# Kernel tuning notes

Hardware: AMD Instinct MI355X
Metric: run time of the kernel (lower is better)

## Reference

```python
import jax, jax.numpy as jnp
import numpy as np

B, K2, C, H, W = 8, 9, 1, 256, 1216


def setup_inputs() -> dict:
    key = jax.random.key(0)
    k1, k2 = jax.random.split(key)
    affinity = jax.random.normal(k1, (B, K2, H, W), dtype=jnp.float32)
    feature = jax.random.normal(k2, (B, C, H, W), dtype=jnp.float32)
    return {"affinity": affinity, "feature": feature, "times": 24}


def reference(affinity, feature, times):
    # affinity: [B, 9, H, W]; feature: [B, C, H, W]
    b, k2, h, w = affinity.shape
    a_abs = jnp.abs(affinity)
    a_norm = a_abs / a_abs.sum(axis=1, keepdims=True)  # per-pixel normalized weights [B,9,H,W]

    def step(feat, _):
        fp = jnp.pad(feat, ((0, 0), (0, 0), (1, 1), (1, 1)))  # 3x3 stencil, pad=1
        # Stack the 9 shifted views: [B, 9, C, H, W] (row-major over 3x3 window,
        # matching index = pad_h*3 + pad_w in the torch loop)
        shifts = jnp.stack(
            [fp[:, :, i:i + h, j:j + w] for i in range(3) for j in range(3)],
            axis=1,
        )
        out = jnp.einsum('bncij,bnij->bcij', shifts, a_norm)
        return out, None

    feat, _ = jax.lax.scan(step, feature, None, length=times)
    return feat
```

## Files before the change

### kernel.cpp

```cpp
#include <hip/hip_runtime.h>

#define BB 8
#define HH 256
#define WW 1216
#define TIMES 24

#define KF 4
#define TSZ 26
#define FSZ 34
#define NT 512
#define NFPIX (FSZ*FSZ)
#define TGX 47
#define TGY 10
#define NTILES (TGX*TGY)

#define WRECD 4096
#define WBYTES (WRECD*4)
#define WCHUNKS (WBYTES/256)

static const size_t HW = (size_t)HH * WW;
#define DEQ (1.0f/65535.0f)

typedef float f32x2 __attribute__((ext_vector_type(2)));

#define LDS_BARRIER() do { asm volatile("s_waitcnt lgkmcnt(0)" ::: "memory"); \
                           __builtin_amdgcn_s_barrier(); } while (0)

__device__ __forceinline__ unsigned lds_off(const void* p) {
    return (unsigned)(size_t)(const __attribute__((address_space(3))) void*)p;
}

__device__ __forceinline__ void gload_lds4(const unsigned int* g, void* l) {
    __builtin_amdgcn_global_load_lds(
        (const __attribute__((address_space(1))) void*)g,
        (__attribute__((address_space(3))) void*)l, 4, 0, 0);
}

#define STEPV(BC, o0, o1) do {                                                        \
    unsigned _ab = lds_off((BC) + tb0);                                               \
    f32x2 _v0,_v1,_v2,_v3,_v4,_v5;                                                    \
    asm volatile("ds_read2_b32 %0, %1 offset0:0   offset1:1"  : "=v"(_v0) : "v"(_ab));\
    asm volatile("ds_read2_b32 %0, %1 offset0:2   offset1:34" : "=v"(_v1) : "v"(_ab));\
    asm volatile("ds_read2_b32 %0, %1 offset0:35  offset1:36" : "=v"(_v2) : "v"(_ab));\
    asm volatile("ds_read2_b32 %0, %1 offset0:68  offset1:69" : "=v"(_v3) : "v"(_ab));\
    asm volatile("ds_read2_b32 %0, %1 offset0:70  offset1:102": "=v"(_v4) : "v"(_ab));\
    asm volatile("ds_read2_b32 %0, %1 offset0:103 offset1:104": "=v"(_v5) : "v"(_ab));\
    asm volatile("s_waitcnt lgkmcnt(0)" ::: "memory");                                \
    __builtin_amdgcn_sched_barrier(0);                                                \
    float _t00=_v0.x,_t01=_v0.y,_t02=_v1.x;                                           \
    float _t10=_v1.y,_t11=_v2.x,_t12=_v2.y;                                           \
    float _t20=_v3.x,_t21=_v3.y,_t22=_v4.x;                                           \
    float _t30=_v4.y,_t31=_v5.x,_t32=_v5.y;                                           \
    (o0) = w0[0]*_t00+w0[1]*_t01+w0[2]*_t02 + w0[3]*_t10+w0[4]*_t11+w0[5]*_t12        \
         + w0[6]*_t20+w0[7]*_t21+w0[8]*_t22;                                          \
    (o1) = w1[0]*_t10+w1[1]*_t11+w1[2]*_t12 + w1[3]*_t20+w1[4]*_t21+w1[5]*_t22        \
         + w1[6]*_t30+w1[7]*_t31+w1[8]*_t32;                                          \
} while (0)

#define STORE2(BN) do {                                                               \
    asm volatile("ds_write2_b32 %0, %1, %2 offset0:0 offset1:34"                      \
        :: "v"(lds_off((BN) + cw0)), "v"(r0), "v"(r1) : "memory");                    \
} while (0)

template <bool FIRST>
__global__ __launch_bounds__(NT, 4) void fused4_kernel(unsigned int* __restrict__ wq,
                                                       const float* __restrict__ aff,
                                                       const float* __restrict__ src,
                                                       float* __restrict__ dst) {
    __shared__ float S[NFPIX], P[NFPIX], Q[NFPIX];
    __shared__ unsigned int Wl[2][WRECD];

    const int t    = threadIdx.x;
    const int wv   = t >> 6;
    const int lane = t & 63;
    const int tile = blockIdx.x;
    const int ty   = tile / TGX, tx = tile - ty * TGX;
    const int x0   = tx * TSZ,   y0 = ty * TSZ;

    const int wx  = t & 31;
    const int wy0 = (t >> 5) * 2;
    const int gx  = x0 - (KF - 1) + wx;
    const int gy0 = y0 - (KF - 1) + wy0;
    const int gy1 = gy0 + 1;
    const bool in0 = (unsigned)gy0 < (unsigned)HH && (unsigned)gx < (unsigned)WW;
    const bool in1 = (unsigned)gy1 < (unsigned)HH && (unsigned)gx < (unsigned)WW;
    const long woff0 = (long)gy0 * WW + gx;
    const long woff1 = (long)gy1 * WW + gx;
    const int  tb0 = wy0 * FSZ + wx;
    const int  cw0 = (wy0 + 1) * FSZ + (wx + 1);
    const int  widx = (t >> 5) * 32 + (t & 31);

    int foff[3]; bool fok[3];
#pragma unroll
    for (int r = 0; r < 3; ++r) {
        int p  = t + r * NT;
        int fy = p / FSZ, fx = p - fy * FSZ;
        int gfy = y0 - KF + fy, gfx = x0 - KF + fx;
        fok[r]  = (p < NFPIX) && (unsigned)gfy < (unsigned)HH && (unsigned)gfx < (unsigned)WW;
        foff[r] = gfy * WW + gfx;
    }

#pragma unroll
    for (int r = 0; r < 3; ++r) {
        int p = t + r * NT;
        if (p < NFPIX) { P[p] = 0.0f; Q[p] = 0.0f; }
    }

    float a0[9], a1[9];
    if (!FIRST) {
        const unsigned int* w32 = wq + (size_t)(tile * BB) * WRECD;
        for (int c = wv; c < WCHUNKS; c += 8)
            gload_lds4(w32 + c * 64 + lane, (char*)&Wl[0][0] + c * 256);
    } else {
#pragma unroll
        for (int n = 0; n < 9; ++n) {
            a0[n] = in0 ? aff[woff0 + (long)n * (long)HW] : 0.0f;
            a1[n] = in1 ? aff[woff1 + (long)n * (long)HW] : 0.0f;
        }
    }
#pragma unroll
    for (int r = 0; r < 3; ++r) {
        int p = t + r * NT;
        if (p < NFPIX) S[p] = fok[r] ? src[foff[r]] : 0.0f;
    }
    __syncthreads();

    for (int b = 0; b < BB; ++b) {
        const int cur = b & 1;
        float w0[9], w1[9];
        if (!FIRST) {
            unsigned s0i = 0, s1i = 0;
#pragma unroll
            for (int n = 0; n < 8; ++n) {
                unsigned u  = Wl[cur][n * 512 + widx];
                unsigned lo = u & 0xffffu, hi = u >> 16;
                w0[n] = (float)lo * DEQ;
                w1[n] = (float)hi * DEQ;
                s0i += lo; s1i += hi;
            }
            unsigned q80 = in0 ? (65535u - s0i) : 0u;
            unsigned q81 = in1 ? (65535u - s1i) : 0u;
            w0[8] = (float)q80 * DEQ;
            w1[8] = (float)q81 * DEQ;
        } else {
            int qi0[9], qi1[9];
            {
                float s0 = 0.0f, s1 = 0.0f;
#pragma unroll
                for (int n = 0; n < 9; ++n) {
                    a0[n] = fabsf(a0[n]); s0 += a0[n];
                    a1[n] = fabsf(a1[n]); s1 += a1[n];
                }
                float sc0 = in0 ? (65535.0f / s0) : 0.0f;
                float sc1 = in1 ? (65535.0f / s1) : 0.0f;
                int tot0 = 0, tot1 = 0, m0 = 0, m1 = 0;
                float vm0 = a0[0], vm1 = a1[0];
#pragma unroll
                for (int n = 0; n < 9; ++n) {
                    qi0[n] = (int)(a0[n] * sc0 + 0.5f); tot0 += qi0[n];
                    qi1[n] = (int)(a1[n] * sc1 + 0.5f); tot1 += qi1[n];
                    if (a0[n] > vm0) { vm0 = a0[n]; m0 = n; }
                    if (a1[n] > vm1) { vm1 = a1[n]; m1 = n; }
                }
                int d0 = 65535 - tot0, d1 = 65535 - tot1;
#pragma unroll
                for (int n = 0; n < 9; ++n) {
                    qi0[n] += (in0 && n == m0) ? d0 : 0;
                    qi1[n] += (in1 && n == m1) ? d1 : 0;
                }
            }
            unsigned int* rec = wq + (size_t)(tile * BB + b) * WRECD;
#pragma unroll
            for (int n = 0; n < 8; ++n)
                rec[n * 512 + widx] = (unsigned)qi0[n] | ((unsigned)qi1[n] << 16);
#pragma unroll
            for (int n = 0; n < 9; ++n) {
                w0[n] = (float)qi0[n] * DEQ;
                w1[n] = (float)qi1[n] * DEQ;
            }
        }

        const bool pf = (b + 1 < BB);
        float fn[3], an0[9], an1[9];
        if (pf) {
            if (!FIRST) {
                const unsigned int* w32 =
                    wq + (size_t)(tile * BB + b + 1) * WRECD;
                for (int c = wv; c < WCHUNKS; c += 8)
                    gload_lds4(w32 + c * 64 + lane,
                               (char*)&Wl[cur ^ 1][0] + c * 256);
            } else {
                const float* ap = aff + (size_t)(b + 1) * 9 * HW;
#pragma unroll
                for (int n = 0; n < 9; ++n) {
                    an0[n] = in0 ? ap[woff0 + (long)n * (long)HW] : 0.0f;
                    an1[n] = in1 ? ap[woff1 + (long)n * (long)HW] : 0.0f;
                }
            }
            const float* sp = src + (size_t)(b + 1) * HW;
#pragma unroll
            for (int r = 0; r < 3; ++r) fn[r] = fok[r] ? sp[foff[r]] : 0.0f;
        }
        __builtin_amdgcn_sched_barrier(0);

        float r0, r1;
        STEPV(S, r0, r1);
        STORE2(P);
        LDS_BARRIER();
        STEPV(P, r0, r1);
        STORE2(Q);
        LDS_BARRIER();
        if (pf) {
#pragma unroll
            for (int r = 0; r < 3; ++r) {
                int p = t + r * NT;
                if (p < NFPIX) S[p] = fn[r];
            }
        }
        STEPV(Q, r0, r1);
        STORE2(P);
        LDS_BARRIER();
        STEPV(P, r0, r1);

        if (FIRST && pf) {
#pragma unroll
            for (int n = 0; n < 9; ++n) { a0[n] = an0[n]; a1[n] = an1[n]; }
        }

        asm volatile("s_waitcnt vmcnt(0)" ::: "memory");
        LDS_BARRIER();

        const size_t base = (size_t)b * HW;
        if ((unsigned)(wx - (KF - 1)) < (unsigned)TSZ) {
            if ((unsigned)(wy0     - (KF - 1)) < (unsigned)TSZ && in0)
                dst[base + (size_t)gy0 * WW + gx] = r0;
            if ((unsigned)(wy0 + 1 - (KF - 1)) < (unsigned)TSZ && in1)
                dst[base + (size_t)gy1 * WW + gx] = r1;
        }
    }
}

extern "C" void kernel_launch(void* const* d_in, const int* in_sizes, int n_in,
                              void* d_out, int out_size, void* d_ws, size_t ws_size,
                              hipStream_t stream) {
    const float* affinity = (const float*)d_in[0];
    const float* feature  = (const float*)d_in[1];

    unsigned int* wq = (unsigned int*)d_ws;
    float* bufA = (float*)((char*)d_ws + (size_t)NTILES * BB * WBYTES);
    float* bufO = (float*)d_out;

    fused4_kernel<true><<<dim3(NTILES), dim3(NT), 0, stream>>>(
        wq, affinity, feature, bufA);

    const float* src = bufA;
    for (int l = 1; l < TIMES / KF; ++l) {
        float* dst = (l & 1) ? bufO : bufA;
        fused4_kernel<false><<<dim3(NTILES), dim3(NT), 0, stream>>>(
            wq, affinity, src, dst);
        src = dst;
    }
}
```

Measured before the change: 159.2 us.

## Use 2x2 pixel-per-thread steady kernel with 256 threads and wider LDS reads

Splits the templated kernel into a first-pass kernel (unchanged, 512 threads) and a new steady-state kernel where each of 256 threads computes a 2x2 pixel quad. The steady kernel loads stencil neighbourhoods with ds_read2_b64 and unpacks quantized weights with ds_read_b64, so overlapping window values are shared and fewer LDS instructions are issued per output. It raises register pressure (four 9-weight arrays) and halves threads per block, with launch bounds lowered to 2 blocks per CU, which may reduce latency hiding.

```diff
diff --git a/kernel.cpp b/kernel.cpp
--- a/kernel.cpp
+++ b/kernel.cpp
@@ -8,7 +8,8 @@
 #define KF 4
 #define TSZ 26
 #define FSZ 34
-#define NT 512
+#define NTF 512
+#define NTS 256
 #define NFPIX (FSZ*FSZ)
 #define TGX 47
 #define TGY 10
@@ -22,6 +23,8 @@
 #define DEQ (1.0f/65535.0f)
 
 typedef float f32x2 __attribute__((ext_vector_type(2)));
+typedef float f32x4 __attribute__((ext_vector_type(4)));
+typedef unsigned int u32x2 __attribute__((ext_vector_type(2)));
 
 #define LDS_BARRIER() do { asm volatile("s_waitcnt lgkmcnt(0)" ::: "memory"); \
                            __builtin_amdgcn_s_barrier(); } while (0)
@@ -62,17 +65,13 @@
         :: "v"(lds_off((BN) + cw0)), "v"(r0), "v"(r1) : "memory");                    \
 } while (0)
 
-template <bool FIRST>
-__global__ __launch_bounds__(NT, 4) void fused4_kernel(unsigned int* __restrict__ wq,
+__global__ __launch_bounds__(NTF, 4) void fused4_first(unsigned int* __restrict__ wq,
                                                        const float* __restrict__ aff,
                                                        const float* __restrict__ src,
                                                        float* __restrict__ dst) {
     __shared__ float S[NFPIX], P[NFPIX], Q[NFPIX];
-    __shared__ unsigned int Wl[2][WRECD];
 
     const int t    = threadIdx.x;
-    const int wv   = t >> 6;
-    const int lane = t & 63;
     const int tile = blockIdx.x;
     const int ty   = tile / TGX, tx = tile - ty * TGX;
     const int x0   = tx * TSZ,   y0 = ty * TSZ;
@@ -93,7 +92,7 @@
     int foff[3]; bool fok[3];
 #pragma unroll
     for (int r = 0; r < 3; ++r) {
-        int p  = t + r * NT;
+        int p  = t + r * NTF;
         int fy = p / FSZ, fx = p - fy * FSZ;
         int gfy = y0 - KF + fy, gfx = x0 - KF + fx;
         fok[r]  = (p < NFPIX) && (unsigned)gfy < (unsigned)HH && (unsigned)gfx < (unsigned)WW;
@@ -102,72 +101,49 @@
 
 #pragma unroll
     for (int r = 0; r < 3; ++r) {
-        int p = t + r * NT;
+        int p = t + r * NTF;
         if (p < NFPIX) { P[p] = 0.0f; Q[p] = 0.0f; }
     }
 
     float a0[9], a1[9];
-    if (!FIRST) {
-        const unsigned int* w32 = wq + (size_t)(tile * BB) * WRECD;
-        for (int c = wv; c < WCHUNKS; c += 8)
-            gload_lds4(w32 + c * 64 + lane, (char*)&Wl[0][0] + c * 256);
-    } else {
-#pragma unroll
-        for (int n = 0; n < 9; ++n) {
-            a0[n] = in0 ? aff[woff0 + (long)n * (long)HW] : 0.0f;
-            a1[n] = in1 ? aff[woff1 + (long)n * (long)HW] : 0.0f;
-        }
+#pragma unroll
+    for (int n = 0; n < 9; ++n) {
+        a0[n] = in0 ? aff[woff0 + (long)n * (long)HW] : 0.0f;
+        a1[n] = in1 ? aff[woff1 + (long)n * (long)HW] : 0.0f;
     }
 #pragma unroll
     for (int r = 0; r < 3; ++r) {
-        int p = t + r * NT;
+        int p = t + r * NTF;
         if (p < NFPIX) S[p] = fok[r] ? src[foff[r]] : 0.0f;
     }
     __syncthreads();
 
     for (int b = 0; b < BB; ++b) {
-        const int cur = b & 1;
         float w0[9], w1[9];
-        if (!FIRST) {
-            unsigned s0i = 0, s1i = 0;
-#pragma unroll
-            for (int n = 0; n < 8; ++n) {
-                unsigned u  = Wl[cur][n * 512 + widx];
-                unsigned lo = u & 0xffffu, hi = u >> 16;
-                w0[n] = (float)lo * DEQ;
-                w1[n] = (float)hi * DEQ;
-                s0i += lo; s1i += hi;
-            }
-            unsigned q80 = in0 ? (65535u - s0i) : 0u;
-            unsigned q81 = in1 ? (65535u - s1i) : 0u;
-            w0[8] = (float)q80 * DEQ;
-            w1[8] = (float)q81 * DEQ;
-        } else {
+        {
             int qi0[9], qi1[9];
-            {
-                float s0 = 0.0f, s1 = 0.0f;
-#pragma unroll
-                for (int n = 0; n < 9; ++n) {
-                    a0[n] = fabsf(a0[n]); s0 += a0[n];
-                    a1[n] = fabsf(a1[n]); s1 += a1[n];
-                }
-                float sc0 = in0 ? (65535.0f / s0) : 0.0f;
-                float sc1 = in1 ? (65535.0f / s1) : 0.0f;
-                int tot0 = 0, tot1 = 0, m0 = 0, m1 = 0;
-                float vm0 = a0[0], vm1 = a1[0];
-#pragma unroll
-                for (int n = 0; n < 9; ++n) {
-                    qi0[n] = (int)(a0[n] * sc0 + 0.5f); tot0 += qi0[n];
-                    qi1[n] = (int)(a1[n] * sc1 + 0.5f); tot1 += qi1[n];
-                    if (a0[n] > vm0) { vm0 = a0[n]; m0 = n; }
-                    if (a1[n] > vm1) { vm1 = a1[n]; m1 = n; }
-                }
-                int d0 = 65535 - tot0, d1 = 65535 - tot1;
-#pragma unroll
-                for (int n = 0; n < 9; ++n) {
-                    qi0[n] += (in0 && n == m0) ? d0 : 0;
-                    qi1[n] += (in1 && n == m1) ? d1 : 0;
-                }
+            float s0 = 0.0f, s1 = 0.0f;
+#pragma unroll
+            for (int n = 0; n < 9; ++n) {
+                a0[n] = fabsf(a0[n]); s0 += a0[n];
+                a1[n] = fabsf(a1[n]); s1 += a1[n];
+            }
+            float sc0 = in0 ? (65535.0f / s0) : 0.0f;
+            float sc1 = in1 ? (65535.0f / s1) : 0.0f;
+            int tot0 = 0, tot1 = 0, m0 = 0, m1 = 0;
+            float vm0 = a0[0], vm1 = a1[0];
+#pragma unroll
+            for (int n = 0; n < 9; ++n) {
+                qi0[n] = (int)(a0[n] * sc0 + 0.5f); tot0 += qi0[n];
+                qi1[n] = (int)(a1[n] * sc1 + 0.5f); tot1 += qi1[n];
+                if (a0[n] > vm0) { vm0 = a0[n]; m0 = n; }
+                if (a1[n] > vm1) { vm1 = a1[n]; m1 = n; }
+            }
+            int d0 = 65535 - tot0, d1 = 65535 - tot1;
+#pragma unroll
+            for (int n = 0; n < 9; ++n) {
+                qi0[n] += (in0 && n == m0) ? d0 : 0;
+                qi1[n] += (in1 && n == m1) ? d1 : 0;
             }
             unsigned int* rec = wq + (size_t)(tile * BB + b) * WRECD;
 #pragma unroll
@@ -183,19 +159,11 @@
         const bool pf = (b + 1 < BB);
         float fn[3], an0[9], an1[9];
         if (pf) {
-            if (!FIRST) {
-                const unsigned int* w32 =
-                    wq + (size_t)(tile * BB + b + 1) * WRECD;
-                for (int c = wv; c < WCHUNKS; c += 8)
-                    gload_lds4(w32 + c * 64 + lane,
-                               (char*)&Wl[cur ^ 1][0] + c * 256);
-            } else {
-                const float* ap = aff + (size_t)(b + 1) * 9 * HW;
-#pragma unroll
-                for (int n = 0; n < 9; ++n) {
-                    an0[n] = in0 ? ap[woff0 + (long)n * (long)HW] : 0.0f;
-                    an1[n] = in1 ? ap[woff1 + (long)n * (long)HW] : 0.0f;
-                }
+            const float* ap = aff + (size_t)(b + 1) * 9 * HW;
+#pragma unroll
+            for (int n = 0; n < 9; ++n) {
+                an0[n] = in0 ? ap[woff0 + (long)n * (long)HW] : 0.0f;
+                an1[n] = in1 ? ap[woff1 + (long)n * (long)HW] : 0.0f;
             }
             const float* sp = src + (size_t)(b + 1) * HW;
 #pragma unroll
@@ -204,29 +172,22 @@
         __builtin_amdgcn_sched_barrier(0);
 
         float r0, r1;
-        STEPV(S, r0, r1);
-        STORE2(P);
-        LDS_BARRIER();
+        STEPV(S, r0, r1); STORE2(P); LDS_BARRIER();
+        STEPV(P, r0, r1); STORE2(Q); LDS_BARRIER();
+        if (pf) {
+#pragma unroll
+            for (int r = 0; r < 3; ++r) {
+                int p = t + r * NTF;
+                if (p < NFPIX) S[p] = fn[r];
+            }
+        }
+        STEPV(Q, r0, r1); STORE2(P); LDS_BARRIER();
         STEPV(P, r0, r1);
-        STORE2(Q);
-        LDS_BARRIER();
-        if (pf) {
-#pragma unroll
-            for (int r = 0; r < 3; ++r) {
-                int p = t + r * NT;
-                if (p < NFPIX) S[p] = fn[r];
-            }
-        }
-        STEPV(Q, r0, r1);
-        STORE2(P);
-        LDS_BARRIER();
-        STEPV(P, r0, r1);
-
-        if (FIRST && pf) {
+
+        if (pf) {
 #pragma unroll
             for (int n = 0; n < 9; ++n) { a0[n] = an0[n]; a1[n] = an1[n]; }
         }
-
         asm volatile("s_waitcnt vmcnt(0)" ::: "memory");
         LDS_BARRIER();
 
@@ -240,6 +201,162 @@
     }
 }
 
+#define STEPQ(BC, R00, R01, R10, R11) do {                                            \
+    unsigned _ab = lds_off((BC) + tb0);                                               \
+    f32x4 _a,_b,_c,_d;                                                                \
+    asm volatile("ds_read2_b64 %0, %1 offset0:0  offset1:1"  : "=v"(_a) : "v"(_ab));  \
+    asm volatile("ds_read2_b64 %0, %1 offset0:17 offset1:18" : "=v"(_b) : "v"(_ab));  \
+    asm volatile("ds_read2_b64 %0, %1 offset0:34 offset1:35" : "=v"(_c) : "v"(_ab));  \
+    asm volatile("ds_read2_b64 %0, %1 offset0:51 offset1:52" : "=v"(_d) : "v"(_ab));  \
+    asm volatile("s_waitcnt lgkmcnt(0)" ::: "memory");                                \
+    __builtin_amdgcn_sched_barrier(0);                                                \
+    R00 = w00[0]*_a.x + w00[1]*_a.y + w00[2]*_a.z                                     \
+        + w00[3]*_b.x + w00[4]*_b.y + w00[5]*_b.z                                     \
+        + w00[6]*_c.x + w00[7]*_c.y + w00[8]*_c.z;                                    \
+    R01 = w01[0]*_a.y + w01[1]*_a.z + w01[2]*_a.w                                     \
+        + w01[3]*_b.y + w01[4]*_b.z + w01[5]*_b.w                                     \
+        + w01[6]*_c.y + w01[7]*_c.z + w01[8]*_c.w;                                    \
+    R10 = w10[0]*_b.x + w10[1]*_b.y + w10[2]*_b.z                                     \
+        + w10[3]*_c.x + w10[4]*_c.y + w10[5]*_c.z                                     \
+        + w10[6]*_d.x + w10[7]*_d.y + w10[8]*_d.z;                                    \
+    R11 = w11[0]*_b.y + w11[1]*_b.z + w11[2]*_b.w                                     \
+        + w11[3]*_c.y + w11[4]*_c.z + w11[5]*_c.w                                     \
+        + w11[6]*_d.y + w11[7]*_d.z + w11[8]*_d.w;                                    \
+} while (0)
+
+#define STOREQ(BN) do {                                                               \
+    unsigned _wa = lds_off((BN) + cw0);                                               \
+    asm volatile("ds_write2_b32 %0, %1, %2 offset0:0  offset1:1"                      \
+        :: "v"(_wa), "v"(r00), "v"(r01) : "memory");                                  \
+    asm volatile("ds_write2_b32 %0, %1, %2 offset0:34 offset1:35"                     \
+        :: "v"(_wa), "v"(r10), "v"(r11) : "memory");                                  \
+} while (0)
+
+#define WRD(OFF, DST) \
+    asm volatile("ds_read_b64 %0, %1 offset:" #OFF : "=v"(DST) : "v"(_wb));
+
+__global__ __launch_bounds__(NTS, 2) void fused4_steady(const unsigned int* __restrict__ wq,
+                                                        const float* __restrict__ src,
+                                                        float* __restrict__ dst) {
+    __shared__ float S[NFPIX], P[NFPIX], Q[NFPIX];
+    __shared__ unsigned int Wl[2][WRECD];
+
+    const int t    = threadIdx.x;
+    const int wv   = t >> 6;
+    const int lane = t & 63;
+    const int tile = blockIdx.x;
+    const int ty   = tile / TGX, tx = tile - ty * TGX;
+    const int x0   = tx * TSZ,   y0 = ty * TSZ;
+
+    const int qx  = t & 15, qy = t >> 4;
+    const int wxA = qx * 2, wyA = qy * 2;
+    const int gxA = x0 - (KF - 1) + wxA;
+    const int gyA = y0 - (KF - 1) + wyA;
+    const bool iny0 = (unsigned)gyA       < (unsigned)HH;
+    const bool iny1 = (unsigned)(gyA + 1) < (unsigned)HH;
+    const bool inx0 = (unsigned)gxA       < (unsigned)WW;
+    const bool inx1 = (unsigned)(gxA + 1) < (unsigned)WW;
+    const bool in00 = iny0 && inx0, in01 = iny0 && inx1;
+    const bool in10 = iny1 && inx0, in11 = iny1 && inx1;
+    const int  tb0 = wyA * FSZ + wxA;
+    const int  cw0 = (wyA + 1) * FSZ + (wxA + 1);
+    const int  qbase = qy * 32 + 2 * qx;
+
+    int foff[5]; bool fok[5];
+#pragma unroll
+    for (int r = 0; r < 5; ++r) {
+        int p  = t + r * NTS;
+        int fy = p / FSZ, fx = p - fy * FSZ;
+        int gfy = y0 - KF + fy, gfx = x0 - KF + fx;
+        fok[r]  = (p < NFPIX) && (unsigned)gfy < (unsigned)HH && (unsigned)gfx < (unsigned)WW;
+        foff[r] = gfy * WW + gfx;
+    }
+
+#pragma unroll
+    for (int r = 0; r < 5; ++r) {
+        int p = t + r * NTS;
+        if (p < NFPIX) { P[p] = 0.0f; Q[p] = 0.0f; }
+    }
+
+    {
+        const unsigned int* w32 = wq + (size_t)(tile * BB) * WRECD;
+        for (int c = wv; c < WCHUNKS; c += 4)
+            gload_lds4(w32 + c * 64 + lane, (char*)&Wl[0][0] + c * 256);
+    }
+#pragma unroll
+    for (int r = 0; r < 5; ++r) {
+        int p = t + r * NTS;
+        if (p < NFPIX) S[p] = fok[r] ? src[foff[r]] : 0.0f;
+    }
+    __syncthreads();
+
+    for (int b = 0; b < BB; ++b) {
+        const int cur = b & 1;
+
+        float w00[9], w01[9], w10[9], w11[9];
+        {
+            unsigned _wb = lds_off(&Wl[cur][qbase]);
+            u32x2 d0,d1,d2,d3,d4,d5,d6,d7;
+            WRD(0,     d0) WRD(2048,  d1) WRD(4096,  d2) WRD(6144,  d3)
+            WRD(8192,  d4) WRD(10240, d5) WRD(12288, d6) WRD(14336, d7)
+            asm volatile("s_waitcnt lgkmcnt(0)" ::: "memory");
+            __builtin_amdgcn_sched_barrier(0);
+            unsigned s00 = 0, s01 = 0, s10 = 0, s11 = 0;
+#define UNP(N, DD) { unsigned _x = (DD).x, _y = (DD).y;                        \
+            unsigned l0 = _x & 0xffffu, h0 = _x >> 16;                         \
+            unsigned l1 = _y & 0xffffu, h1 = _y >> 16;                         \
+            w00[N] = (float)l0 * DEQ; w10[N] = (float)h0 * DEQ;                \
+            w01[N] = (float)l1 * DEQ; w11[N] = (float)h1 * DEQ;                \
+            s00 += l0; s10 += h0; s01 += l1; s11 += h1; }
+            UNP(0,d0) UNP(1,d1) UNP(2,d2) UNP(3,d3)
+            UNP(4,d4) UNP(5,d5) UNP(6,d6) UNP(7,d7)
+#undef UNP
+            w00[8] = (float)(in00 ? 65535u - s00 : 0u) * DEQ;
+            w01[8] = (float)(in01 ? 65535u - s01 : 0u) * DEQ;
+            w10[8] = (float)(in10 ? 65535u - s10 : 0u) * DEQ;
+            w11[8] = (float)(in11 ? 65535u - s11 : 0u) * DEQ;
+        }
+
+        const bool pf = (b + 1 < BB);
+        float fn[5];
+        if (pf) {
+            const unsigned int* w32 = wq + (size_t)(tile * BB + b + 1) * WRECD;
+            for (int c = wv; c < WCHUNKS; c += 4)
+                gload_lds4(w32 + c * 64 + lane, (char*)&Wl[cur ^ 1][0] + c * 256);
+            const float* sp = src + (size_t)(b + 1) * HW;
+#pragma unroll
+            for (int r = 0; r < 5; ++r) fn[r] = fok[r] ? sp[foff[r]] : 0.0f;
+        }
+        __builtin_amdgcn_sched_barrier(0);
+
+        float r00, r01, r10, r11;
+        STEPQ(S, r00, r01, r10, r11); STOREQ(P); LDS_BARRIER();
+        STEPQ(P, r00, r01, r10, r11); STOREQ(Q); LDS_BARRIER();
+        if (pf) {
+#pragma unroll
+            for (int r = 0; r < 5; ++r) {
+                int p = t + r * NTS;
+                if (p < NFPIX) S[p] = fn[r];
+            }
+        }
+        STEPQ(Q, r00, r01, r10, r11); STOREQ(P); LDS_BARRIER();
+        STEPQ(P, r00, r01, r10, r11);
+
+        asm volatile("s_waitcnt vmcnt(0)" ::: "memory");
+        LDS_BARRIER();
+
+        const size_t base = (size_t)b * HW;
+        const bool tx0 = (unsigned)(wxA     - (KF - 1)) < (unsigned)TSZ;
+        const bool tx1 = (unsigned)(wxA + 1 - (KF - 1)) < (unsigned)TSZ;
+        const bool ty0 = (unsigned)(wyA     - (KF - 1)) < (unsigned)TSZ;
+        const bool ty1 = (unsigned)(wyA + 1 - (KF - 1)) < (unsigned)TSZ;
+        if (ty0 && tx0 && in00) dst[base + (size_t)gyA * WW + gxA]           = r00;
+        if (ty0 && tx1 && in01) dst[base + (size_t)gyA * WW + gxA + 1]       = r01;
+        if (ty1 && tx0 && in10) dst[base + (size_t)(gyA + 1) * WW + gxA]     = r10;
+        if (ty1 && tx1 && in11) dst[base + (size_t)(gyA + 1) * WW + gxA + 1] = r11;
+    }
+}
+
 extern "C" void kernel_launch(void* const* d_in, const int* in_sizes, int n_in,
                               void* d_out, int out_size, void* d_ws, size_t ws_size,
                               hipStream_t stream) {
@@ -250,14 +367,14 @@
     float* bufA = (float*)((char*)d_ws + (size_t)NTILES * BB * WBYTES);
     float* bufO = (float*)d_out;
 
-    fused4_kernel<true><<<dim3(NTILES), dim3(NT), 0, stream>>>(
+    fused4_first<<<dim3(NTILES), dim3(NTF), 0, stream>>>(
         wq, affinity, feature, bufA);
 
     const float* src = bufA;
     for (int l = 1; l < TIMES / KF; ++l) {
         float* dst = (l & 1) ? bufO : bufA;
-        fused4_kernel<false><<<dim3(NTILES), dim3(NT), 0, stream>>>(
-            wq, affinity, src, dst);
+        fused4_steady<<<dim3(NTILES), dim3(NTS), 0, stream>>>(
+            wq, src, dst);
         src = dst;
     }
 }
```

New measurement: 183.2 us. +15.0%, slower.
